# Kernel tuning notes

Hardware: AMD Instinct MI355X
Metric: run time of the kernel (lower is better)

Reference implementation:

```python
import jax, jax.numpy as jnp
import numpy as np

D_MODEL = 1024
N_HEADS = 16
D_K = D_MODEL // N_HEADS
LN_EPS = 1e-5


def setup_inputs() -> dict:
    key = jax.random.key(0)
    ks = jax.random.split(key, 12)
    B, S, D = 4, 2048, D_MODEL
    s = 1.0 / np.sqrt(D)
    return {
        "Q": jax.random.normal(ks[0], (B, S, D), jnp.float32),
        "K": jax.random.normal(ks[1], (B, S, D), jnp.float32),
        "V": jax.random.normal(ks[2], (B, S, D), jnp.float32),
        "W_q": jax.random.normal(ks[3], (D, D), jnp.float32) * s,
        "b_q": jnp.zeros((D,), jnp.float32),
        "W_k": jax.random.normal(ks[4], (D, D), jnp.float32) * s,
        "b_k": jnp.zeros((D,), jnp.float32),
        "W_v": jax.random.normal(ks[5], (D, D), jnp.float32) * s,
        "b_v": jnp.zeros((D,), jnp.float32),
        "W_o": jax.random.normal(ks[6], (D, D), jnp.float32) * s,
        "b_o": jnp.zeros((D,), jnp.float32),
        "ln_gamma": jnp.ones((D,), jnp.float32),
        "ln_beta": jnp.zeros((D,), jnp.float32),
    }


def _split_heads(x):  # (B,S,D) -> (B,H,S,Dk)
    B, S, _ = x.shape
    return x.reshape(B, S, N_HEADS, D_K).transpose(0, 2, 1, 3)


def reference(Q, K, V, W_q, b_q, W_k, b_k, W_v, b_v, W_o, b_o, ln_gamma, ln_beta):
    # Linear projections (torch Linear: x @ W^T + b)
    q = Q @ W_q.T + b_q  # (B,S,D) -- also the residual in this module
    k = K @ W_k.T + b_k
    v = V @ W_v.T + b_v
    qh, kh, vh = _split_heads(q), _split_heads(k), _split_heads(v)
    scale = 1.0 / jnp.sqrt(jnp.float32(D_K))
    scores = jnp.einsum("bhqd,bhkd->bhqk", qh, kh) * scale
    attn = jax.nn.softmax(scores, axis=-1)  # dropout = identity (eval)
    ctx = jnp.einsum("bhqk,bhkd->bhqd", attn, vh)
    B, H, S, Dk = ctx.shape
    ctx = ctx.transpose(0, 2, 1, 3).reshape(B, S, H * Dk)  # (B,S,D)
    out = ctx @ W_o.T + b_o
    # residual uses projected Q (module quirk), then LayerNorm
    x = out + q
    mu = jnp.mean(x, axis=-1, keepdims=True)
    var = jnp.mean((x - mu) ** 2, axis=-1, keepdims=True)
    return (x - mu) * jax.lax.rsqrt(var + LN_EPS) * ln_gamma + ln_beta
```

## Files before the change

kernel.cpp:

```cpp
#include <hip/hip_runtime.h>
#include <hip/hip_bf16.h>
#include <stdint.h>

#define D_MODEL 1024
#define NH 16
#define DKH 64
#define NBATCH 4
#define SEQ 2048
#define NROWS (NBATCH*SEQ)

typedef __bf16 bf16;
typedef __bf16 bf16x8 __attribute__((ext_vector_type(8)));
typedef __bf16 bf16x4 __attribute__((ext_vector_type(4)));
typedef float f32x4 __attribute__((ext_vector_type(4)));

static __device__ __forceinline__ f32x4 fzero4() {
  f32x4 z; z[0] = 0.f; z[1] = 0.f; z[2] = 0.f; z[3] = 0.f; return z;
}

static __device__ __forceinline__ float fast_exp2(float x) {
  return __builtin_amdgcn_exp2f(x);
}

static __device__ __forceinline__ void gload16(const bf16* g, bf16* lds) {
  __builtin_amdgcn_global_load_lds(
      (const __attribute__((address_space(1))) uint32_t*)(uintptr_t)g,
      (__attribute__((address_space(3))) uint32_t*)(uintptr_t)lds,
      16, 0, 0);
}

__global__ __launch_bounds__(256) void cvt_w4(const float* __restrict__ a,
                                              const float* __restrict__ b,
                                              const float* __restrict__ c,
                                              const float* __restrict__ d,
                                              bf16* __restrict__ out) {
  const float* srcs[4] = {a, b, c, d};
  const float* s = srcs[blockIdx.y];
  int i = blockIdx.x * 256 + threadIdx.x;
  float4 v = ((const float4*)s)[i];
  bf16x4 o;
  o[0] = (bf16)v.x; o[1] = (bf16)v.y; o[2] = (bf16)v.z; o[3] = (bf16)v.w;
  ((bf16x4*)out)[blockIdx.y * (D_MODEL * D_MODEL / 4) + i] = o;
}

__global__ __launch_bounds__(256) void gemm_qkv(const float* __restrict__ Qin,
                                                const float* __restrict__ Kin,
                                                const float* __restrict__ Vin,
                                                const bf16* __restrict__ Wall,
                                                const float* __restrict__ bq,
                                                const float* __restrict__ bk,
                                                const float* __restrict__ bv,
                                                bf16* __restrict__ qbf,
                                                bf16* __restrict__ kpb,
                                                bf16* __restrict__ vtb) {
  __shared__ __align__(16) bf16 As[2][128 * 64];
  __shared__ __align__(16) bf16 Bs[2][128 * 64];
  const int orig = blockIdx.x + ((blockIdx.y + (blockIdx.z << 6)) << 3);
  const int work = ((orig & 7) * 192) + (orig >> 3);
  const int bn = work & 7;
  const int bm = (work >> 3) & 63;
  const int z = work >> 9;

  const float* A = z == 0 ? Qin : (z == 1 ? Kin : Vin);
  const bf16* B = Wall + (size_t)z * D_MODEL * D_MODEL;
  const float* bias = z == 0 ? bq : (z == 1 ? bk : bv);
  const int N = D_MODEL;

  const int t = threadIdx.x, w = t >> 6, l = t & 63;
  const int wm = w >> 1, wn = w & 1;
  const int lr = l & 15, g = l >> 4;
  const int rowA0 = bm * 128, colB0 = bn * 128;

  const int c8 = l & 7;
  const int rbase = l >> 3;

  f32x4 aE0[4], aE1[4];
  f32x4 aO0[4], aO1[4];

#define LOADA(K0, R0, R1)                                                     \
  {                                                                           \
    _Pragma("unroll")                                                         \
    for (int i = 0; i < 4; i++) {                                             \
      int r = (w * 4 + i) * 8 + rbase;                                        \
      const float* p = A + (size_t)(rowA0 + r) * D_MODEL + (K0) + c8 * 8;     \
      R0[i] = *(const f32x4*)p;                                               \
      R1[i] = *(const f32x4*)(p + 4);                                         \
    }                                                                         \
  }
#define WRITEA(BUF, R0, R1)                                                   \
  {                                                                           \
    _Pragma("unroll")                                                         \
    for (int i = 0; i < 4; i++) {                                             \
      int r = (w * 4 + i) * 8 + rbase;                                        \
      bf16x8 o;                                                               \
      _Pragma("unroll")                                                       \
      for (int j = 0; j < 4; j++) { o[j] = (bf16)R0[i][j]; o[4 + j] = (bf16)R1[i][j]; } \
      *(bf16x8*)((char*)As[BUF] + r * 128 + ((c8 * 16) ^ ((r & 7) << 4))) = o; \
    }                                                                         \
  }
#define STAGEB(K0, BUF)                                                       \
  {                                                                           \
    _Pragma("unroll")                                                         \
    for (int i = 0; i < 4; i++) {                                             \
      int r = (w * 4 + i) * 8 + rbase;                                        \
      int cb = (c8 * 16) ^ ((r & 7) << 4);                                    \
      gload16(B + (size_t)(colB0 + r) * D_MODEL + (K0) + (cb >> 1),           \
              &Bs[BUF][(w * 4 + i) * 512]);                                   \
    }                                                                         \
  }
#define COMPUTE(BUF)                                                          \
  {                                                                           \
    _Pragma("unroll")                                                         \
    for (int kk = 0; kk < 2; kk++) {                                          \
      bf16x8 av[4], bv4[4];                                                   \
      _Pragma("unroll")                                                       \
      for (int m = 0; m < 4; m++) {                                           \
        int row = wm * 64 + m * 16 + lr;                                      \
        int off = row * 128 + ((kk * 64 + g * 16) ^ ((row & 7) << 4));        \
        av[m] = *(const bf16x8*)((const char*)As[BUF] + off);                 \
      }                                                                       \
      _Pragma("unroll")                                                       \
      for (int n = 0; n < 4; n++) {                                           \
        int row = wn * 64 + n * 16 + lr;                                      \
        int off = row * 128 + ((kk * 64 + g * 16) ^ ((row & 7) << 4));        \
        bv4[n] = *(const bf16x8*)((const char*)Bs[BUF] + off);                \
      }                                                                       \
      _Pragma("unroll")                                                       \
      for (int m = 0; m < 4; m++)                                             \
        _Pragma("unroll")                                                     \
        for (int n = 0; n < 4; n++)                                           \
          acc[m][n] = __builtin_amdgcn_mfma_f32_16x16x32_bf16(av[m], bv4[n], acc[m][n], 0, 0, 0); \
    }                                                                         \
  }

  f32x4 acc[4][4];
#pragma unroll
  for (int m = 0; m < 4; m++)
#pragma unroll
    for (int n = 0; n < 4; n++) acc[m][n] = fzero4();

  LOADA(0, aE0, aE1); STAGEB(0, 0);
  LOADA(64, aO0, aO1); STAGEB(64, 1);
  asm volatile("s_waitcnt vmcnt(12)" ::: "memory");
  WRITEA(0, aE0, aE1);
  asm volatile("s_waitcnt lgkmcnt(0)" ::: "memory");
  __builtin_amdgcn_s_barrier();
  asm volatile("" ::: "memory");

  for (int it = 0; it < 8; ++it) {
    const int kt0 = 2 * it;
    if (it < 7) LOADA((kt0 + 2) * 64, aE0, aE1);
    COMPUTE(0);
    if (it < 7) asm volatile("s_waitcnt vmcnt(8)" ::: "memory");
    else        asm volatile("s_waitcnt vmcnt(0)" ::: "memory");
    WRITEA(1, aO0, aO1);
    asm volatile("s_waitcnt lgkmcnt(0)" ::: "memory");
    __builtin_amdgcn_s_barrier();
    asm volatile("" ::: "memory");
    if (it < 7) STAGEB((kt0 + 2) * 64, 0);
    if (it < 7) {
      LOADA((kt0 + 3) * 64, aO0, aO1);
      COMPUTE(1);
      asm volatile("s_waitcnt vmcnt(8)" ::: "memory");
      WRITEA(0, aE0, aE1);
      asm volatile("s_waitcnt lgkmcnt(0)" ::: "memory");
      __builtin_amdgcn_s_barrier();
      asm volatile("" ::: "memory");
      STAGEB((kt0 + 3) * 64, 1);
    } else {
      COMPUTE(1);
    }
  }
#undef LOADA
#undef WRITEA
#undef STAGEB
#undef COMPUTE

  if (z == 2) {
#pragma unroll
    for (int n = 0; n < 4; n++) {
      int col = colB0 + wn * 64 + n * 16 + lr;
      float bc = bias[col];
      int hh = col >> 6, dh = col & 63;
#pragma unroll
      for (int m = 0; m < 4; m++) {
        int row = rowA0 + wm * 64 + m * 16 + g * 4;
        int bb = row >> 11;
        int ss = row & 2047;
        int pos = (ss & ~31) + g * 8 + (m & 1) * 4;
        bf16x4 o;
#pragma unroll
        for (int j = 0; j < 4; j++) o[j] = (bf16)(acc[m][n][j] + bc);
        *(bf16x4*)(vtb + (((size_t)(bb * NH + hh)) * DKH + dh) * SEQ + pos) = o;
      }
    }
  } else {
    bf16* Cb = z == 0 ? qbf : kpb;
    const float bscale = z == 0 ? 0.180336880111f : 1.0f;
#pragma unroll
    for (int n = 0; n < 4; n++) {
      int col = colB0 + wn * 64 + n * 16 + lr;
      float bc = bias[col];
#pragma unroll
      for (int m = 0; m < 4; m++) {
#pragma unroll
        for (int j = 0; j < 4; j++) {
          int row = rowA0 + wm * 64 + m * 16 + g * 4 + j;
          Cb[(size_t)row * N + col] = (bf16)((acc[m][n][j] + bc) * bscale);
        }
      }
    }
  }
}

#define STAGE_G(K0, BUF)                                                      \
  {                                                                           \
    _Pragma("unroll")                                                         \
    for (int i = 0; i < 4; i++) {                                             \
      int r = (w * 4 + i) * 8 + (l >> 3);                                     \
      int cb = ((l & 7) * 16) ^ ((r & 7) << 4);                               \
      gload16(A + (size_t)(rowA0 + r) * D_MODEL + (K0) + (cb >> 1),           \
              &As[BUF][(w * 4 + i) * 512]);                                   \
      gload16(B + (size_t)(colB0 + r) * D_MODEL + (K0) + (cb >> 1),           \
              &Bs[BUF][(w * 4 + i) * 512]);                                   \
    }                                                                         \
  }

__global__ __launch_bounds__(256) void gemm_o(const bf16* __restrict__ A,
                                              const bf16* __restrict__ B,
                                              const float* __restrict__ bias,
                                              float* __restrict__ Cf) {
  __shared__ __align__(16) bf16 As[2][128 * 64];
  __shared__ __align__(16) bf16 Bs[2][128 * 64];
  const int orig = blockIdx.x + (blockIdx.y << 3);
  const int work = ((orig & 7) * 64) + (orig >> 3);
  const int bn = work & 7, bm = work >> 3;
  const int t = threadIdx.x, w = t >> 6, l = t & 63;
  const int wm = w >> 1, wn = w & 1;
  const int lr = l & 15, g = l >> 4;
  const int rowA0 = bm * 128, colB0 = bn * 128;
  const int N = D_MODEL;

  f32x4 acc[4][4];
#pragma unroll
  for (int m = 0; m < 4; m++)
#pragma unroll
    for (int n = 0; n < 4; n++) acc[m][n] = fzero4();

  STAGE_G(0, 0);
  STAGE_G(64, 1);
  int cur = 0;
  for (int kt = 0; kt < 16; ++kt) {
    if (kt < 15) asm volatile("s_waitcnt vmcnt(8)" ::: "memory");
    else         asm volatile("s_waitcnt vmcnt(0)" ::: "memory");
    __builtin_amdgcn_s_barrier();
    asm volatile("" ::: "memory");
#pragma unroll
    for (int kk = 0; kk < 2; kk++) {
      bf16x8 av[4], bv4[4];
#pragma unroll
      for (int m = 0; m < 4; m++) {
        int row = wm * 64 + m * 16 + lr;
        int off = row * 128 + ((kk * 64 + g * 16) ^ ((row & 7) << 4));
        av[m] = *(const bf16x8*)((const char*)As[cur] + off);
      }
#pragma unroll
      for (int n = 0; n < 4; n++) {
        int row = wn * 64 + n * 16 + lr;
        int off = row * 128 + ((kk * 64 + g * 16) ^ ((row & 7) << 4));
        bv4[n] = *(const bf16x8*)((const char*)Bs[cur] + off);
      }
#pragma unroll
      for (int m = 0; m < 4; m++)
#pragma unroll
        for (int n = 0; n < 4; n++)
          acc[m][n] = __builtin_amdgcn_mfma_f32_16x16x32_bf16(av[m], bv4[n], acc[m][n], 0, 0, 0);
    }
    asm volatile("s_waitcnt lgkmcnt(0)" ::: "memory");
    __builtin_amdgcn_s_barrier();
    if (kt < 14) STAGE_G((kt + 2) * 64, cur);
    cur ^= 1;
  }

#pragma unroll
  for (int n = 0; n < 4; n++) {
    int col = colB0 + wn * 64 + n * 16 + lr;
    float bc = bias[col];
#pragma unroll
    for (int m = 0; m < 4; m++) {
#pragma unroll
      for (int j = 0; j < 4; j++) {
        int row = rowA0 + wm * 64 + m * 16 + g * 4 + j;
        Cf[(size_t)row * N + col] = acc[m][n][j] + bc;
      }
    }
  }
}

__global__ __launch_bounds__(256, 4) void attn_fwd(const bf16* __restrict__ Qp,
                                                   const bf16* __restrict__ Kp,
                                                   const bf16* __restrict__ Vt,
                                                   bf16* __restrict__ Ctx) {
  __shared__ __align__(16) bf16 Ks[2][64 * 64];
  __shared__ __align__(16) bf16 Vs[2][64 * 64];
  const int bid0 = blockIdx.x;
  const int bid = ((bid0 & 7) << 7) | (bid0 >> 3);
  const int qt = bid & 15;
  const int h = (bid >> 4) & 15;
  const int b = bid >> 8;
  const int w = threadIdx.x >> 6, l = threadIdx.x & 63;
  const int lr = l & 15, g = l >> 4;
  const int q0 = qt * 128 + w * 32;

  const size_t qkBase = ((size_t)b * SEQ) * D_MODEL + h * DKH;
  const size_t vtBase = ((size_t)(b * NH + h)) * DKH * SEQ;
  const bf16* Kg = Kp + qkBase;
  const bf16* Vg = Vt + vtBase;

  const int sr = w * 8 + (l >> 3);
  const int scb = (l & 7) * 16;

  bf16x8 qf[2][2];
#pragma unroll
  for (int f = 0; f < 2; f++)
#pragma unroll
    for (int kk = 0; kk < 2; kk++)
      qf[f][kk] = *(const bf16x8*)(Qp + qkBase + (size_t)(q0 + f * 16 + lr) * D_MODEL + kk * 32 + g * 8);

  bf16x8 vone;
#pragma unroll
  for (int j = 0; j < 8; j++) vone[j] = (bf16)1.0f;

  f32x4 ctx[2][5];
#pragma unroll
  for (int f = 0; f < 2; f++)
#pragma unroll
    for (int n = 0; n < 5; n++) ctx[f][n] = fzero4();

#define STAGE(T, BUF)                                                         \
  {                                                                           \
    const int _s0 = (T) * 64;                                                 \
    _Pragma("unroll")                                                         \
    for (int i = 0; i < 2; i++) {                                             \
      int r = i * 32 + sr;                                                    \
      int cb = scb ^ ((r & 7) << 4);                                          \
      gload16(Kg + (size_t)(_s0 + r) * D_MODEL + (cb >> 1),                   \
              &Ks[BUF][i * 2048 + w * 512]);                                  \
      gload16(Vg + (size_t)r * SEQ + _s0 + (cb >> 1),                         \
              &Vs[BUF][i * 2048 + w * 512]);                                  \
    }                                                                         \
  }

  STAGE(0, 0);
  int cur = 0;
  for (int t = 0; t < SEQ / 64; ++t) {
    if (t + 1 < SEQ / 64) {
      STAGE(t + 1, cur ^ 1);
      asm volatile("s_waitcnt vmcnt(4)" ::: "memory");
    } else {
      asm volatile("s_waitcnt vmcnt(0)" ::: "memory");
    }
    __builtin_amdgcn_s_barrier();
    asm volatile("" ::: "memory");

#pragma unroll
    for (int ss = 0; ss < 2; ++ss) {
      bf16x8 ka[2][2];
#pragma unroll
      for (int hf = 0; hf < 2; hf++) {
        int row = ss * 32 + hf * 16 + lr;
#pragma unroll
        for (int kk = 0; kk < 2; kk++) {
          int off = row * 128 + ((kk * 64 + g * 16) ^ ((row & 7) << 4));
          ka[hf][kk] = *(const bf16x8*)((const char*)Ks[cur] + off);
        }
      }
      bf16x8 vb[4];
#pragma unroll
      for (int n = 0; n < 4; n++) {
        int row = n * 16 + lr;
        int off = row * 128 + ((ss * 64 + g * 16) ^ ((row & 7) << 4));
        vb[n] = *(const bf16x8*)((const char*)Vs[cur] + off);
      }

#pragma unroll
      for (int f = 0; f < 2; f++) {
        f32x4 sc[2];
        __builtin_amdgcn_s_setprio(1);
#pragma unroll
        for (int hf = 0; hf < 2; hf++) {
          f32x4 tt = fzero4();
          tt = __builtin_amdgcn_mfma_f32_16x16x32_bf16(ka[hf][0], qf[f][0], tt, 0, 0, 0);
          tt = __builtin_amdgcn_mfma_f32_16x16x32_bf16(ka[hf][1], qf[f][1], tt, 0, 0, 0);
          sc[hf] = tt;
        }
        __builtin_amdgcn_s_setprio(0);
        float p[8];
#pragma unroll
        for (int hf = 0; hf < 2; hf++)
#pragma unroll
          for (int j = 0; j < 4; j++)
            p[hf * 4 + j] = fast_exp2(sc[hf][j]);
        bf16x8 pa;
#pragma unroll
        for (int j = 0; j < 8; j++) pa[j] = (bf16)p[j];
        __builtin_amdgcn_s_setprio(1);
#pragma unroll
        for (int n = 0; n < 4; n++)
          ctx[f][n] = __builtin_amdgcn_mfma_f32_16x16x32_bf16(pa, vb[n], ctx[f][n], 0, 0, 0);
        ctx[f][4] = __builtin_amdgcn_mfma_f32_16x16x32_bf16(pa, vone, ctx[f][4], 0, 0, 0);
        __builtin_amdgcn_s_setprio(0);
      }
    }
    asm volatile("" ::: "memory");
    __builtin_amdgcn_s_barrier();
    cur ^= 1;
  }
#undef STAGE

#pragma unroll
  for (int f = 0; f < 2; f++) {
#pragma unroll
    for (int j = 0; j < 4; j++) {
      float lj = 1.0f / ctx[f][4][j];
      int s = q0 + f * 16 + g * 4 + j;
      size_t base = ((size_t)b * SEQ + s) * D_MODEL + h * DKH;
#pragma unroll
      for (int n = 0; n < 4; n++)
        Ctx[base + n * 16 + lr] = (bf16)(ctx[f][n][j] * lj);
    }
  }
}

__global__ __launch_bounds__(256) void ln_res(const float* __restrict__ O,
                                              const bf16* __restrict__ Rb,
                                              const float* __restrict__ gam,
                                              const float* __restrict__ bet,
                                              float* __restrict__ out) {
  const int row = blockIdx.x, t = threadIdx.x;
  const size_t idx = (size_t)row * 256 + t;
  const float4 o = ((const float4*)O)[idx];
  const bf16x4 rb = ((const bf16x4*)Rb)[idx];
  const float rs = 5.545177444479562f;
  float x0 = o.x + (float)rb[0] * rs, x1 = o.y + (float)rb[1] * rs;
  float x2 = o.z + (float)rb[2] * rs, x3 = o.w + (float)rb[3] * rs;
  float s = x0 + x1 + x2 + x3;
  float q = x0 * x0 + x1 * x1 + x2 * x2 + x3 * x3;
#pragma unroll
  for (int off = 32; off >= 1; off >>= 1) {
    s += __shfl_xor(s, off);
    q += __shfl_xor(q, off);
  }
  __shared__ float red[8];
  const int wid = t >> 6;
  if ((t & 63) == 0) { red[wid] = s; red[4 + wid] = q; }
  __syncthreads();
  s = red[0] + red[1] + red[2] + red[3];
  q = red[4] + red[5] + red[6] + red[7];
  const float mu = s * (1.f / 1024.f);
  const float rinv = rsqrtf(q * (1.f / 1024.f) - mu * mu + 1e-5f);
  const float4 g4 = ((const float4*)gam)[t];
  const float4 b4 = ((const float4*)bet)[t];
  float4 y;
  y.x = (x0 - mu) * rinv * g4.x + b4.x;
  y.y = (x1 - mu) * rinv * g4.y + b4.y;
  y.z = (x2 - mu) * rinv * g4.z + b4.z;
  y.w = (x3 - mu) * rinv * g4.w + b4.w;
  ((float4*)out)[idx] = y;
}

extern "C" void kernel_launch(void* const* d_in, const int* in_sizes, int n_in,
                              void* d_out, int out_size, void* d_ws, size_t ws_size,
                              hipStream_t stream) {
  const float* Q   = (const float*)d_in[0];
  const float* Kx  = (const float*)d_in[1];
  const float* V   = (const float*)d_in[2];
  const float* Wq  = (const float*)d_in[3];
  const float* bq  = (const float*)d_in[4];
  const float* Wk  = (const float*)d_in[5];
  const float* bk  = (const float*)d_in[6];
  const float* Wv  = (const float*)d_in[7];
  const float* bv  = (const float*)d_in[8];
  const float* Wo  = (const float*)d_in[9];
  const float* bo  = (const float*)d_in[10];
  const float* gam = (const float*)d_in[11];
  const float* bet = (const float*)d_in[12];
  float* out = (float*)d_out;

  char* ws = (char*)d_ws;
  const size_t MB = 1ull << 20;
  bf16* wall = (bf16*)(ws);
  bf16* qbf  = (bf16*)(ws + 8 * MB);
  bf16* kpb  = (bf16*)(ws + 24 * MB);
  bf16* vtb  = (bf16*)(ws + 40 * MB);
  bf16* ctx  = (bf16*)(ws + 56 * MB);
  float* attnout = (float*)(ws + 72 * MB);

  const int nW4 = D_MODEL * D_MODEL / 4;
  dim3 cb(256);

  cvt_w4<<<dim3(nW4 / 256, 4), cb, 0, stream>>>(Wq, Wk, Wv, Wo, wall);

  gemm_qkv<<<dim3(8, 64, 3), cb, 0, stream>>>(Q, Kx, V, wall, bq, bk, bv, qbf, kpb, vtb);

  attn_fwd<<<NBATCH * NH * 16, cb, 0, stream>>>(qbf, kpb, vtb, ctx);

  gemm_o<<<dim3(8, 64), cb, 0, stream>>>(ctx, wall + 3ull * D_MODEL * D_MODEL, bo, attnout);
  ln_res<<<NROWS, cb, 0, stream>>>(attnout, qbf, gam, bet, out);
}
```

Baseline: 186.9 us.

## Deepen QKV GEMM pipeline to three stages with triple-buffered B tiles

Restructures the QKV projection GEMM main loop into a fully unrolled, three-stage software pipeline. The bf16 weight tiles are now triple-buffered in LDS, and three fp32 A register sets keep global loads two to three k-tiles ahead of compute. The aim is to hide global-memory latency for the fp32 activation loads and the weight DMA behind the MFMA work. In exchange it uses more LDS (an extra 16KB buffer) and more VGPRs for the extra A registers, which may reduce occupancy or cause spills. It also relies on hand-tuned vmcnt wait counts that must exactly match the number of outstanding loads.

```diff
diff --git a/kernel.cpp b/kernel.cpp
--- a/kernel.cpp
+++ b/kernel.cpp
@@ -28,6 +28,8 @@
       (__attribute__((address_space(3))) uint32_t*)(uintptr_t)lds,
       16, 0, 0);
 }
+
+#define FENCE asm volatile("" ::: "memory")
 
 __global__ __launch_bounds__(256) void cvt_w4(const float* __restrict__ a,
                                               const float* __restrict__ b,
@@ -54,7 +56,7 @@
                                                 bf16* __restrict__ kpb,
                                                 bf16* __restrict__ vtb) {
   __shared__ __align__(16) bf16 As[2][128 * 64];
-  __shared__ __align__(16) bf16 Bs[2][128 * 64];
+  __shared__ __align__(16) bf16 Bs[3][128 * 64];
   const int orig = blockIdx.x + ((blockIdx.y + (blockIdx.z << 6)) << 3);
   const int work = ((orig & 7) * 192) + (orig >> 3);
   const int bn = work & 7;
@@ -74,8 +76,9 @@
   const int c8 = l & 7;
   const int rbase = l >> 3;
 
-  f32x4 aE0[4], aE1[4];
-  f32x4 aO0[4], aO1[4];
+  f32x4 a00[4], a01[4];
+  f32x4 a10[4], a11[4];
+  f32x4 a20[4], a21[4];
 
 #define LOADA(K0, R0, R1)                                                     \
   {                                                                           \
@@ -87,7 +90,7 @@
       R1[i] = *(const f32x4*)(p + 4);                                         \
     }                                                                         \
   }
-#define WRITEA(BUF, R0, R1)                                                   \
+#define WRITEA(R0, R1, AB)                                                    \
   {                                                                           \
     _Pragma("unroll")                                                         \
     for (int i = 0; i < 4; i++) {                                             \
@@ -95,20 +98,20 @@
       bf16x8 o;                                                               \
       _Pragma("unroll")                                                       \
       for (int j = 0; j < 4; j++) { o[j] = (bf16)R0[i][j]; o[4 + j] = (bf16)R1[i][j]; } \
-      *(bf16x8*)((char*)As[BUF] + r * 128 + ((c8 * 16) ^ ((r & 7) << 4))) = o; \
+      *(bf16x8*)((char*)As[AB] + r * 128 + ((c8 * 16) ^ ((r & 7) << 4))) = o; \
     }                                                                         \
   }
-#define STAGEB(K0, BUF)                                                       \
+#define STAGEB(K0, BB)                                                        \
   {                                                                           \
     _Pragma("unroll")                                                         \
     for (int i = 0; i < 4; i++) {                                             \
       int r = (w * 4 + i) * 8 + rbase;                                        \
       int cb = (c8 * 16) ^ ((r & 7) << 4);                                    \
       gload16(B + (size_t)(colB0 + r) * D_MODEL + (K0) + (cb >> 1),           \
-              &Bs[BUF][(w * 4 + i) * 512]);                                   \
+              &Bs[BB][(w * 4 + i) * 512]);                                    \
     }                                                                         \
   }
-#define COMPUTE(BUF)                                                          \
+#define COMPUTE(AB, BB)                                                       \
   {                                                                           \
     _Pragma("unroll")                                                         \
     for (int kk = 0; kk < 2; kk++) {                                          \
@@ -117,13 +120,13 @@
       for (int m = 0; m < 4; m++) {                                           \
         int row = wm * 64 + m * 16 + lr;                                      \
         int off = row * 128 + ((kk * 64 + g * 16) ^ ((row & 7) << 4));        \
-        av[m] = *(const bf16x8*)((const char*)As[BUF] + off);                 \
+        av[m] = *(const bf16x8*)((const char*)As[AB] + off);                  \
       }                                                                       \
       _Pragma("unroll")                                                       \
       for (int n = 0; n < 4; n++) {                                           \
         int row = wn * 64 + n * 16 + lr;                                      \
         int off = row * 128 + ((kk * 64 + g * 16) ^ ((row & 7) << 4));        \
-        bv4[n] = *(const bf16x8*)((const char*)Bs[BUF] + off);                \
+        bv4[n] = *(const bf16x8*)((const char*)Bs[BB] + off);                 \
       }                                                                       \
       _Pragma("unroll")                                                       \
       for (int m = 0; m < 4; m++)                                             \
@@ -132,6 +135,19 @@
           acc[m][n] = __builtin_amdgcn_mfma_f32_16x16x32_bf16(av[m], bv4[n], acc[m][n], 0, 0, 0); \
     }                                                                         \
   }
+#define FULLSTEP(KT, SLa, SLb, SWa, SWb, AW, AC, BC, BSB, VMC)                \
+  {                                                                           \
+    if ((KT) < 14) { STAGEB(((KT) + 2) * 64, BSB); }                          \
+    FENCE;                                                                    \
+    if ((KT) < 13) { LOADA(((KT) + 3) * 64, SLa, SLb); }                      \
+    FENCE;                                                                    \
+    COMPUTE(AC, BC);                                                          \
+    asm volatile("s_waitcnt vmcnt(" #VMC ")" ::: "memory");                   \
+    WRITEA(SWa, SWb, AW);                                                     \
+    asm volatile("s_waitcnt lgkmcnt(0)" ::: "memory");                        \
+    __builtin_amdgcn_s_barrier();                                             \
+    FENCE;                                                                    \
+  }
 
   f32x4 acc[4][4];
 #pragma unroll
@@ -139,42 +155,39 @@
 #pragma unroll
     for (int n = 0; n < 4; n++) acc[m][n] = fzero4();
 
-  LOADA(0, aE0, aE1); STAGEB(0, 0);
-  LOADA(64, aO0, aO1); STAGEB(64, 1);
-  asm volatile("s_waitcnt vmcnt(12)" ::: "memory");
-  WRITEA(0, aE0, aE1);
+  LOADA(0, a00, a01); FENCE;
+  STAGEB(0, 0); FENCE;
+  LOADA(64, a10, a11); FENCE;
+  STAGEB(64, 1); FENCE;
+  LOADA(128, a20, a21); FENCE;
+  asm volatile("s_waitcnt vmcnt(20)" ::: "memory");
+  WRITEA(a00, a01, 0);
   asm volatile("s_waitcnt lgkmcnt(0)" ::: "memory");
   __builtin_amdgcn_s_barrier();
-  asm volatile("" ::: "memory");
-
-  for (int it = 0; it < 8; ++it) {
-    const int kt0 = 2 * it;
-    if (it < 7) LOADA((kt0 + 2) * 64, aE0, aE1);
-    COMPUTE(0);
-    if (it < 7) asm volatile("s_waitcnt vmcnt(8)" ::: "memory");
-    else        asm volatile("s_waitcnt vmcnt(0)" ::: "memory");
-    WRITEA(1, aO0, aO1);
-    asm volatile("s_waitcnt lgkmcnt(0)" ::: "memory");
-    __builtin_amdgcn_s_barrier();
-    asm volatile("" ::: "memory");
-    if (it < 7) STAGEB((kt0 + 2) * 64, 0);
-    if (it < 7) {
-      LOADA((kt0 + 3) * 64, aO0, aO1);
-      COMPUTE(1);
-      asm volatile("s_waitcnt vmcnt(8)" ::: "memory");
-      WRITEA(0, aE0, aE1);
-      asm volatile("s_waitcnt lgkmcnt(0)" ::: "memory");
-      __builtin_amdgcn_s_barrier();
-      asm volatile("" ::: "memory");
-      STAGEB((kt0 + 3) * 64, 1);
-    } else {
-      COMPUTE(1);
-    }
-  }
+  FENCE;
+
+  FULLSTEP( 0,  a00, a01,    a10, a11,    1, 0, 0, 2, 20)
+  FULLSTEP( 1,  a10, a11,    a20, a21,    0, 1, 1, 0, 20)
+  FULLSTEP( 2,  a20, a21,    a00, a01,    1, 0, 2, 1, 20)
+  FULLSTEP( 3,  a00, a01,    a10, a11,    0, 1, 0, 2, 20)
+  FULLSTEP( 4,  a10, a11,    a20, a21,    1, 0, 1, 0, 20)
+  FULLSTEP( 5,  a20, a21,    a00, a01,    0, 1, 2, 1, 20)
+  FULLSTEP( 6,  a00, a01,    a10, a11,    1, 0, 0, 2, 20)
+  FULLSTEP( 7,  a10, a11,    a20, a21,    0, 1, 1, 0, 20)
+  FULLSTEP( 8,  a20, a21,    a00, a01,    1, 0, 2, 1, 20)
+  FULLSTEP( 9,  a00, a01,    a10, a11,    0, 1, 0, 2, 20)
+  FULLSTEP(10,  a10, a11,    a20, a21,    1, 0, 1, 0, 20)
+  FULLSTEP(11,  a20, a21,    a00, a01,    0, 1, 2, 1, 20)
+  FULLSTEP(12,  a00, a01,    a10, a11,    1, 0, 0, 2, 20)
+  FULLSTEP(13,  a10, a11,    a20, a21,    0, 1, 1, 0, 12)
+  FULLSTEP(14,  a20, a21,    a00, a01,    1, 0, 2, 1, 0)
+  COMPUTE(1, 0);
+
 #undef LOADA
 #undef WRITEA
 #undef STAGEB
 #undef COMPUTE
+#undef FULLSTEP
 
   if (z == 2) {
 #pragma unroll
@@ -254,7 +267,7 @@
     if (kt < 15) asm volatile("s_waitcnt vmcnt(8)" ::: "memory");
     else         asm volatile("s_waitcnt vmcnt(0)" ::: "memory");
     __builtin_amdgcn_s_barrier();
-    asm volatile("" ::: "memory");
+    FENCE;
 #pragma unroll
     for (int kk = 0; kk < 2; kk++) {
       bf16x8 av[4], bv4[4];
@@ -361,7 +374,7 @@
       asm volatile("s_waitcnt vmcnt(0)" ::: "memory");
     }
     __builtin_amdgcn_s_barrier();
-    asm volatile("" ::: "memory");
+    FENCE;
 
 #pragma unroll
     for (int ss = 0; ss < 2; ++ss) {
@@ -412,7 +425,7 @@
         __builtin_amdgcn_s_setprio(0);
       }
     }
-    asm volatile("" ::: "memory");
+    FENCE;
     __builtin_amdgcn_s_barrier();
     cur ^= 1;
   }
```

Measured after the change: 203.8 us. 1.09x slower.
